# Performance work log

Measured on AMD Instinct MI355X. Metric: run time of the kernel, lower is better.

The kernel has to match this reference:

```python
import jax, jax.numpy as jnp
import numpy as np

N, E, B = 20000, 60000, 800
H = 64          # node_out_feats
EOUT = 64       # edge_out_feats
D = H + EOUT    # set2set input dim = 128
NT = 138        # n_tasks


def _forward(node_feats, edge_feats, fp_vector, src, dst, gid,
             Wn, bn, We1, be1, We2, be2, Wres, Wgx, bgx, Wgh, bgh,
             Wep, bep,
             Wlx0, Wlh0, bl0, Wlx1, Wlh1, bl1, Wlx2, Wlh2, bl2,
             Wfp, bfp, bn_g, bn_b, bn_m, bn_v,
             Wf1, bf1, Wf2, bf2, Wp, bp):
    # ---- CustomMPNNGNN (dgllife MPNNGNN: proj + NNConv(edge-net) + GRU) ----
    h = jax.nn.relu(node_feats @ Wn + bn)                       # [N,64]
    We = jax.nn.relu(edge_feats @ We1 + be1) @ We2 + be2        # [E,4096]
    We = We.reshape(-1, H, H)                                   # [E,64,64] per-edge weight
    hs = h                                                      # GRU hidden state
    for _ in range(3):
        msg = jnp.einsum('ei,eio->eo', h[src], We)              # edge gather + matvec
        agg = jax.ops.segment_sum(msg, dst, num_segments=N)     # scatter-add to dst
        m = jax.nn.relu(agg + h @ Wres)                         # residual root weight
        gx = m @ Wgx + bgx
        gh = hs @ Wgh + bgh
        xr, xz, xn = jnp.split(gx, 3, axis=-1)
        hr, hz, hn = jnp.split(gh, 3, axis=-1)
        r = jax.nn.sigmoid(xr + hr)
        z = jax.nn.sigmoid(xz + hz)
        n = jnp.tanh(xn + r * hn)
        hs = (1.0 - z) * n + z * hs
        h = hs
    # ---- _internal_readout: gather src node emb + projected edge emb, segment-sum at dst ----
    e_emb = jax.nn.relu(edge_feats @ Wep + bep)                 # [E,64]
    src_msg = jnp.concatenate([h[src], e_emb], axis=1)          # [E,128]
    feat = jax.ops.segment_sum(src_msg, dst, num_segments=N)    # [N,128]
    # ---- Set2Set (3-layer LSTM hidden 128, 6 iterations) ----
    q_star = jnp.zeros((B, 2 * D), feat.dtype)
    hc = [(jnp.zeros((B, D), feat.dtype), jnp.zeros((B, D), feat.dtype)) for _ in range(3)]
    lstm = [(Wlx0, Wlh0, bl0), (Wlx1, Wlh1, bl1), (Wlx2, Wlh2, bl2)]
    for _ in range(6):
        x = q_star
        new_hc = []
        for (Wx, Wh, b), (hl, cl) in zip(lstm, hc):
            g = x @ Wx + hl @ Wh + b                            # [B,512] gates i,f,g,o
            gi, gf, gg, go = jnp.split(g, 4, axis=-1)
            cl = jax.nn.sigmoid(gf) * cl + jax.nn.sigmoid(gi) * jnp.tanh(gg)
            hl = jax.nn.sigmoid(go) * jnp.tanh(cl)
            new_hc.append((hl, cl))
            x = hl
        hc = new_hc
        q = x                                                   # [B,128]
        e = jnp.sum(feat * q[gid], axis=-1)                     # [N]
        emax = jax.ops.segment_max(e, gid, num_segments=B)
        a = jnp.exp(e - emax[gid])
        denom = jax.ops.segment_sum(a, gid, num_segments=B)
        alpha = a / (denom[gid] + 1e-9)
        r = jax.ops.segment_sum(alpha[:, None] * feat, gid, num_segments=B)  # [B,128]
        q_star = jnp.concatenate([q, r], axis=1)                # [B,256]
    # ---- Fingerprint encoder: Linear + BatchNorm1d(eval) + ReLU ----
    fp = fp_vector @ Wfp + bfp
    fp = jax.nn.relu((fp - bn_m) * bn_g * jax.lax.rsqrt(bn_v + 1e-5) + bn_b)  # [B,128]
    # ---- combined FFN (384 -> 300 -> 256) + prediction head ----
    comb = jnp.concatenate([q_star, fp], axis=1)                # [B,384]
    emb = jax.nn.relu(comb @ Wf1 + bf1) @ Wf2 + bf2             # [B,256]
    out = jax.nn.relu(emb) @ Wp + bp                            # [B,138]
    return out


def setup_inputs() -> dict:
    key = jax.random.key(0)
    ks = iter(jax.random.split(key, 64))
    def nrm(shape, s):
        return jax.random.normal(next(ks), shape, jnp.float32) * s
    inp = {}
    inp['node_feats'] = jax.random.normal(next(ks), (N, 134), jnp.float32)
    inp['edge_feats'] = jax.random.uniform(next(ks), (E, 6), jnp.float32)
    inp['fp_vector'] = jax.random.uniform(next(ks), (B, 1024), jnp.float32)
    inp['src'] = jax.random.randint(next(ks), (E,), 0, N)
    inp['dst'] = jax.random.randint(next(ks), (E,), 0, N)
    inp['gid'] = jnp.sort(jax.random.randint(next(ks), (N,), 0, B))
    # MPNN params
    inp['Wn'] = nrm((134, H), 0.08); inp['bn'] = jnp.zeros((H,), jnp.float32)
    inp['We1'] = nrm((6, 128), 0.2); inp['be1'] = jnp.zeros((128,), jnp.float32)
    inp['We2'] = nrm((128, H * H), 0.05); inp['be2'] = jnp.zeros((H * H,), jnp.float32)
    inp['Wres'] = nrm((H, H), 0.1)
    inp['Wgx'] = nrm((H, 3 * H), 0.1); inp['bgx'] = jnp.zeros((3 * H,), jnp.float32)
    inp['Wgh'] = nrm((H, 3 * H), 0.1); inp['bgh'] = jnp.zeros((3 * H,), jnp.float32)
    # edge projection for readout
    inp['Wep'] = nrm((6, EOUT), 0.2); inp['bep'] = jnp.zeros((EOUT,), jnp.float32)
    # Set2Set LSTM (layer0 input 2D=256, layers 1-2 input D=128, hidden D=128)
    inp['Wlx0'] = nrm((2 * D, 4 * D), 0.06); inp['Wlh0'] = nrm((D, 4 * D), 0.06); inp['bl0'] = jnp.zeros((4 * D,), jnp.float32)
    inp['Wlx1'] = nrm((D, 4 * D), 0.06); inp['Wlh1'] = nrm((D, 4 * D), 0.06); inp['bl1'] = jnp.zeros((4 * D,), jnp.float32)
    inp['Wlx2'] = nrm((D, 4 * D), 0.06); inp['Wlh2'] = nrm((D, 4 * D), 0.06); inp['bl2'] = jnp.zeros((4 * D,), jnp.float32)
    # fingerprint encoder
    inp['Wfp'] = nrm((1024, 128), 0.03); inp['bfp'] = jnp.zeros((128,), jnp.float32)
    inp['bn_g'] = jnp.ones((128,), jnp.float32); inp['bn_b'] = jnp.zeros((128,), jnp.float32)
    inp['bn_m'] = jnp.zeros((128,), jnp.float32); inp['bn_v'] = jnp.ones((128,), jnp.float32)
    # combined FFN + prediction head
    inp['Wf1'] = nrm((2 * D + 128, 300), 0.06); inp['bf1'] = jnp.zeros((300,), jnp.float32)
    inp['Wf2'] = nrm((300, 256), 0.06); inp['bf2'] = jnp.zeros((256,), jnp.float32)
    inp['Wp'] = nrm((256, NT), 0.06); inp['bp'] = jnp.zeros((NT,), jnp.float32)
    return inp


def reference(node_feats, edge_feats, fp_vector, src, dst, gid,
              Wn, bn, We1, be1, We2, be2, Wres, Wgx, bgx, Wgh, bgh,
              Wep, bep,
              Wlx0, Wlh0, bl0, Wlx1, Wlh1, bl1, Wlx2, Wlh2, bl2,
              Wfp, bfp, bn_g, bn_b, bn_m, bn_v,
              Wf1, bf1, Wf2, bf2, Wp, bp):
    return _forward(node_feats, edge_feats, fp_vector, src, dst, gid,
                    Wn, bn, We1, be1, We2, be2, Wres, Wgx, bgx, Wgh, bgh,
                    Wep, bep,
                    Wlx0, Wlh0, bl0, Wlx1, Wlh1, bl1, Wlx2, Wlh2, bl2,
                    Wfp, bfp, bn_g, bn_b, bn_m, bn_v,
                    Wf1, bf1, Wf2, bf2, Wp, bp)
```

## Files before the change

### kernel.cpp

```cpp
#include <hip/hip_runtime.h>

typedef short short8 __attribute__((ext_vector_type(8)));
typedef float f32x4  __attribute__((ext_vector_type(4)));
typedef unsigned int u32x4 __attribute__((ext_vector_type(4)));
typedef _Float16 f16x2 __attribute__((ext_vector_type(2)));

#define NN 20000
#define NE 60000
#define NB 800
#define NTASK 138
#define EB 128
#define EPAD 60032

#define O_WX0 0
#define O_WH0 131072
#define O_WX1 196608
#define O_WH1 262144
#define O_WX2 327680
#define O_WH2 393216
#define O_WF1 458752
#define O_WF2 573952
#define O_WP  650752
#define NWB   686080

#if defined(__has_builtin)
#if __has_builtin(__builtin_amdgcn_fdot2)
#define HAVE_DOT2 1
#else
#define HAVE_DOT2 0
#endif
#else
#define HAVE_DOT2 0
#endif

static __device__ __forceinline__ float sigm(float x) { return 1.f / (1.f + expf(-x)); }

static __device__ __forceinline__ unsigned short f2bf(float x) {
    unsigned u = __float_as_uint(x);
    unsigned r = (u + 0x7fffu + ((u >> 16) & 1u)) >> 16;
    return (unsigned short)r;
}
static __device__ __forceinline__ float bf2f(unsigned short b) {
    return __uint_as_float(((unsigned)b) << 16);
}

#if HAVE_DOT2
static __device__ __forceinline__ unsigned short f2w(float x) {
    _Float16 h = (_Float16)x;
    return __builtin_bit_cast(unsigned short, h);
}
static __device__ __forceinline__ float w2f(unsigned short s) {
    return (float)__builtin_bit_cast(_Float16, s);
}
static __device__ __forceinline__ unsigned int pack2f16(float a, float b) {
    unsigned short lo = __builtin_bit_cast(unsigned short, (_Float16)a);
    unsigned short hi = __builtin_bit_cast(unsigned short, (_Float16)b);
    return ((unsigned)hi << 16) | lo;
}
#define BC2(u) __builtin_bit_cast(f16x2, (unsigned int)(u))
#else
static __device__ __forceinline__ unsigned short f2w(float x) { return f2bf(x); }
static __device__ __forceinline__ float w2f(unsigned short s) { return bf2f(s); }
#endif

__global__ void kpre(float* __restrict__ zbase, int nz4,
                     const float* __restrict__ We2, const float* __restrict__ be2,
                     unsigned short* __restrict__ thi,
                     const int* __restrict__ gid, int* __restrict__ seg,
                     const float* __restrict__ fpv, const float* __restrict__ Wfp,
                     const float* __restrict__ bfpv,
                     const float* __restrict__ bng, const float* __restrict__ bnb,
                     const float* __restrict__ bnm, const float* __restrict__ bnv,
                     float* __restrict__ fpb,
                     const float* __restrict__ nf, const float* __restrict__ Wn,
                     const float* __restrict__ bn, float* __restrict__ hf,
                     unsigned short* __restrict__ hb,
                     const float* __restrict__ ef, const float* __restrict__ We1,
                     const float* __restrict__ be1, float* __restrict__ xt,
                     const float* __restrict__ Wlx0, const float* __restrict__ Wlh0,
                     const float* __restrict__ Wlx1, const float* __restrict__ Wlh1,
                     const float* __restrict__ Wlx2, const float* __restrict__ Wlh2,
                     const float* __restrict__ Wf1, const float* __restrict__ Wf2,
                     const float* __restrict__ Wp, unsigned short* __restrict__ wb,
                     int B0, int B1, int B2, int B3, int B4, int B5) {
    __shared__ float st[64 * 65];
    __shared__ float sNF[16 * 134];
    __shared__ float sred[128];
    __shared__ float sW[6 * 128];
    __shared__ float sbv[128];
    const int bid = blockIdx.x, tid = threadIdx.x;
    if (bid < B0) {
        long base = (long)bid * 2048 + tid;
        #pragma unroll
        for (int r = 0; r < 8; ++r) {
            long i = base + r * 256;
            if (i < nz4) reinterpret_cast<f32x4*>(zbase)[i] = f32x4{0.f, 0.f, 0.f, 0.f};
        }
    } else if (bid < B1) {
        int c = bid - B0;
        const float* srcp = (c < 128) ? We2 + (long)c * 4096 : be2;
        for (int idx = tid; idx < 4096; idx += 256) {
            int o = idx & 63, i = idx >> 6;
            st[o * 65 + i] = srcp[idx];
        }
        __syncthreads();
        for (int idx = tid; idx < 4096; idx += 256) {
            int i = idx & 63, o = idx >> 6;
            thi[(long)c * 4096 + idx] = f2bf(st[o * 65 + i]);
        }
    } else if (bid < B2) {
        int b = (bid - B1) * 256 + tid;
        if (b <= NB) {
            int lo = 0, hi = NN;
            while (lo < hi) { int mid = (lo + hi) >> 1; if (gid[mid] < b) lo = mid + 1; else hi = mid; }
            seg[b] = lo;
        }
    } else if (bid < B3) {
        int g = bid - B2;
        int u = tid & 127, half = tid >> 7;
        float acc = half ? 0.f : bfpv[u];
        const float* fr = fpv + (long)g * 1024 + half * 512;
        const float* wr = Wfp + (long)half * 512 * 128;
        for (int k = 0; k < 512; ++k) acc += fr[k] * wr[k * 128 + u];
        if (half) sred[u] = acc;
        __syncthreads();
        if (!half) {
            acc += sred[u];
            float sc = bng[u] / sqrtf(bnv[u] + 1e-5f);
            fpb[(long)g * 128 + u] = fmaxf((acc - bnm[u]) * sc + bnb[u], 0.f);
        }
    } else if (bid < B4) {
        int n0 = (bid - B3) * 16;
        const float* nfb = nf + (long)n0 * 134;
        for (int i = tid; i < 16 * 134; i += 256) sNF[i] = nfb[i];
        __syncthreads();
        int u = tid & 63, jg = tid >> 6;
        float a[4];
        float bv = bn[u];
        #pragma unroll
        for (int jj = 0; jj < 4; ++jj) a[jj] = bv;
        for (int k = 0; k < 134; ++k) {
            float w = Wn[k * 64 + u];
            #pragma unroll
            for (int jj = 0; jj < 4; ++jj) a[jj] += sNF[(jg * 4 + jj) * 134 + k] * w;
        }
        #pragma unroll
        for (int jj = 0; jj < 4; ++jj) {
            long o = (long)(n0 + jg * 4 + jj) * 64 + u;
            float v = fmaxf(a[jj], 0.f);
            hf[o] = v;
            hb[o] = f2bf(v);
        }
    } else if (bid < B5) {
        for (int i = tid; i < 768; i += 256) sW[i] = We1[i];
        if (tid < 128) sbv[tid] = be1[tid];
        __syncthreads();
        int e = (bid - B4) * 256 + tid;
        if (e < NE) {
            float e0 = ef[(long)e * 6 + 0], e1 = ef[(long)e * 6 + 1], e2 = ef[(long)e * 6 + 2];
            float e3 = ef[(long)e * 6 + 3], e4 = ef[(long)e * 6 + 4], e5 = ef[(long)e * 6 + 5];
            for (int c = 0; c < 128; ++c) {
                float a = sbv[c];
                a += e0 * sW[c];       a += e1 * sW[128 + c]; a += e2 * sW[256 + c];
                a += e3 * sW[384 + c]; a += e4 * sW[512 + c]; a += e5 * sW[640 + c];
                xt[(long)c * EPAD + e] = fmaxf(a, 0.f);
            }
        } else if (e < EPAD) {
            for (int c = 0; c < 128; ++c) xt[(long)c * EPAD + e] = 0.f;
        }
    } else {
        int t0 = (bid - B5) * 2048 + tid;
        #pragma unroll
        for (int r = 0; r < 8; ++r) {
            int i = t0 + r * 256;
            if (i >= NWB) break;
            float v;
            if (i < O_WF1) {
                const float* srcp; int base;
                if (i < O_WH0)      { srcp = Wlx0; base = O_WX0; }
                else if (i < O_WX1) { srcp = Wlh0; base = O_WH0; }
                else if (i < O_WH1) { srcp = Wlx1; base = O_WX1; }
                else if (i < O_WX2) { srcp = Wlh1; base = O_WH1; }
                else if (i < O_WH2) { srcp = Wlx2; base = O_WX2; }
                else                { srcp = Wlh2; base = O_WH2; }
                int il = i - base;
                int kb = il >> 12, g = (il >> 3) & 511, kk = il & 7;
                v = srcp[(kb * 8 + kk) * 512 + g];
            }
            else if (i < O_WF2) v = Wf1[i - O_WF1];
            else if (i < O_WP)  v = Wf2[i - O_WF2];
            else                v = Wp[i - O_WP];
            wb[i] = f2w(v);
        }
    }
}

__global__ __launch_bounds__(256) void keinsum(
    const unsigned short* __restrict__ hb,
    const float* __restrict__ hf, const float* __restrict__ Wres,
    const float* __restrict__ xt,
    const unsigned short* __restrict__ thi,
    const int* __restrict__ src, const int* __restrict__ dst,
    float* __restrict__ agg) {
    __shared__ __align__(16) unsigned short sB[3 * 64 * 72];
    __shared__ __align__(16) float sX[3 * EB];
    const int bid = blockIdx.x, tid = threadIdx.x;
    if (bid >= 469) {
        int t = (bid - 469) * 256 + tid;
        int u = t & 63;
        int n0 = (t >> 6) * 8;
        if (n0 >= NN) return;
        float a[8] = {0.f, 0.f, 0.f, 0.f, 0.f, 0.f, 0.f, 0.f};
        for (int k = 0; k < 64; ++k) {
            float w = Wres[k * 64 + u];
            #pragma unroll
            for (int j = 0; j < 8; ++j) a[j] += hf[(long)(n0 + j) * 64 + k] * w;
        }
        #pragma unroll
        for (int j = 0; j < 8; ++j) atomicAdd(&agg[(long)(n0 + j) * 64 + u], a[j]);
        return;
    }
    const int lane = tid & 63, wave = tid >> 6;
    const int m = lane & 15, q = lane >> 4;
    const int eb = bid * EB;
    const int e0 = eb + wave * 32;

    short8 ahi[2][2];
    #pragma unroll
    for (int eg = 0; eg < 2; ++eg) {
        int em = e0 + eg * 16 + m; if (em >= NE) em = NE - 1;
        int sn = src[em];
        ahi[eg][0] = *reinterpret_cast<const short8*>(hb + (long)sn * 64 + q * 8);
        ahi[eg][1] = *reinterpret_cast<const short8*>(hb + (long)sn * 64 + 32 + q * 8);
    }
    float msg[2][4][4];
    #pragma unroll
    for (int eg = 0; eg < 2; ++eg)
        #pragma unroll
        for (int nt = 0; nt < 4; ++nt)
            #pragma unroll
            for (int r = 0; r < 4; ++r) msg[eg][nt][r] = 0.f;

    short8 rB0a, rB0b, rB1a, rB1b;
    float rX0, rX1;

    auto GLOAD0 = [&](int c) {
        const unsigned short* bb = thi + (long)c * 4096;
        rB0a = *reinterpret_cast<const short8*>(bb + tid * 8);
        rB0b = *reinterpret_cast<const short8*>(bb + (tid + 256) * 8);
        rX0 = (tid < EB) ? ((c < 128) ? xt[(long)c * EPAD + eb + tid] : 1.f) : 0.f;
    };
    auto GLOAD1 = [&](int c) {
        const unsigned short* bb = thi + (long)c * 4096;
        rB1a = *reinterpret_cast<const short8*>(bb + tid * 8);
        rB1b = *reinterpret_cast<const short8*>(bb + (tid + 256) * 8);
        rX1 = (tid < EB) ? ((c < 128) ? xt[(long)c * EPAD + eb + tid] : 1.f) : 0.f;
    };
    auto DSW0 = [&](int buf) {
        unsigned short* base = &sB[buf * 4608];
        *reinterpret_cast<short8*>(&base[(tid >> 3) * 72 + (tid & 7) * 8]) = rB0a;
        int u = tid + 256;
        *reinterpret_cast<short8*>(&base[(u >> 3) * 72 + (u & 7) * 8]) = rB0b;
        if (tid < EB) sX[buf * EB + tid] = rX0;
    };
    auto DSW1 = [&](int buf) {
        unsigned short* base = &sB[buf * 4608];
        *reinterpret_cast<short8*>(&base[(tid >> 3) * 72 + (tid & 7) * 8]) = rB1a;
        int u = tid + 256;
        *reinterpret_cast<short8*>(&base[(u >> 3) * 72 + (u & 7) * 8]) = rB1b;
        if (tid < EB) sX[buf * EB + tid] = rX1;
    };
    auto CMP = [&](int buf) {
        const unsigned short* base = &sB[buf * 4608];
        f32x4 xw[2];
        #pragma unroll
        for (int eg = 0; eg < 2; ++eg)
            xw[eg] = *reinterpret_cast<const f32x4*>(&sX[buf * EB + wave * 32 + eg * 16 + q * 4]);
        short8 b0[4], b1[4];
        #pragma unroll
        for (int nt = 0; nt < 4; ++nt) {
            const unsigned short* rp = &base[(nt * 16 + m) * 72 + q * 8];
            b0[nt] = *reinterpret_cast<const short8*>(rp);
            b1[nt] = *reinterpret_cast<const short8*>(rp + 32);
        }
        #pragma unroll
        for (int eg = 0; eg < 2; ++eg)
            #pragma unroll
            for (int nt = 0; nt < 4; ++nt) {
                f32x4 z = {0.f, 0.f, 0.f, 0.f};
                z = __builtin_amdgcn_mfma_f32_16x16x32_bf16(ahi[eg][0], b0[nt], z, 0, 0, 0);
                z = __builtin_amdgcn_mfma_f32_16x16x32_bf16(ahi[eg][1], b1[nt], z, 0, 0, 0);
                #pragma unroll
                for (int r = 0; r < 4; ++r) msg[eg][nt][r] += xw[eg][r] * z[r];
            }
    };

    GLOAD0(0);
    DSW0(0);
    GLOAD1(1);
    int c = 0;
    for (; c + 1 < 129; c += 2) {
        int s = c % 3;
        __syncthreads();
        if (c + 2 < 129) GLOAD0(c + 2);
        DSW1((s + 1) % 3);
        CMP(s);
        __syncthreads();
        if (c + 3 < 129) GLOAD1(c + 3);
        if (c + 2 < 129) DSW0((s + 2) % 3);
        CMP((s + 1) % 3);
    }
    if (c < 129) { __syncthreads(); CMP(c % 3); }

    #pragma unroll
    for (int eg = 0; eg < 2; ++eg)
        #pragma unroll
        for (int r = 0; r < 4; ++r) {
            int e = e0 + eg * 16 + q * 4 + r;
            if (e < NE) {
                int d = dst[e];
                #pragma unroll
                for (int nt = 0; nt < 4; ++nt)
                    atomicAdd(&agg[(long)d * 64 + nt * 16 + m], msg[eg][nt][r]);
            }
        }
}

__global__ void kgruz(const float* __restrict__ agg, const float* __restrict__ h,
                      const float* __restrict__ Wgx, const float* __restrict__ bgx,
                      const float* __restrict__ Wgh, const float* __restrict__ bgh,
                      float* __restrict__ hof, unsigned short* __restrict__ hb,
                      float* __restrict__ aggN) {
    const int bid = blockIdx.x, tid = threadIdx.x;
    if (bid >= 625) {
        long base = (long)(bid - 625) * 2048 + tid;
        #pragma unroll
        for (int r = 0; r < 8; ++r) {
            long i = base + r * 256;
            if (i < 320000) reinterpret_cast<f32x4*>(aggN)[i] = f32x4{0.f, 0.f, 0.f, 0.f};
        }
        return;
    }
    __shared__ float sA[2048], sH[2048];
    const int n0 = bid * 32;
    const float* ab = agg + (long)n0 * 64;
    const float* hrow = h + (long)n0 * 64;
    for (int i = tid; i < 2048; i += 256) { sA[i] = ab[i]; sH[i] = hrow[i]; }
    __syncthreads();
    const int u = tid & 63, jg = tid >> 6;
    float xr[8], xz[8], xn[8], hr[8], hz[8], hn[8];
    float b0 = bgx[u], b1 = bgx[64 + u], b2 = bgx[128 + u];
    float d0 = bgh[u], d1 = bgh[64 + u], d2 = bgh[128 + u];
    #pragma unroll
    for (int j = 0; j < 8; ++j) {
        xr[j] = b0; xz[j] = b1; xn[j] = b2;
        hr[j] = d0; hz[j] = d1; hn[j] = d2;
    }
    for (int k = 0; k < 64; ++k) {
        float w0 = Wgx[k * 192 + u], w1 = Wgx[k * 192 + 64 + u], w2 = Wgx[k * 192 + 128 + u];
        float v0 = Wgh[k * 192 + u], v1 = Wgh[k * 192 + 64 + u], v2 = Wgh[k * 192 + 128 + u];
        #pragma unroll
        for (int j = 0; j < 8; ++j) {
            int n = jg * 8 + j;
            float mk = fmaxf(sA[n * 64 + k], 0.f);
            float hk = sH[n * 64 + k];
            xr[j] += mk * w0; xz[j] += mk * w1; xn[j] += mk * w2;
            hr[j] += hk * v0; hz[j] += hk * v1; hn[j] += hk * v2;
        }
    }
    #pragma unroll
    for (int j = 0; j < 8; ++j) {
        int n = jg * 8 + j;
        float rg = sigm(xr[j] + hr[j]);
        float zg = sigm(xz[j] + hz[j]);
        float ng = tanhf(xn[j] + rg * hn[j]);
        long o = (long)(n0 + n) * 64 + u;
        float hv = (1.f - zg) * ng + zg * sH[n * 64 + u];
        hof[o] = hv;
        hb[o] = f2bf(hv);
    }
}

__global__ void kreadout(const float* __restrict__ h,
                         const float* __restrict__ ef, const float* __restrict__ Wep,
                         const float* __restrict__ bep,
                         const int* __restrict__ src, const int* __restrict__ dst,
                         float* __restrict__ feat) {
    int t = blockIdx.x * blockDim.x + threadIdx.x;
    if (t >= NE * 128) return;
    int e = t >> 7, j = t & 127;
    float v;
    if (j < 64) {
        v = h[(long)src[e] * 64 + j];
    } else {
        int o = j - 64;
        v = bep[o];
        #pragma unroll
        for (int k = 0; k < 6; ++k) v += ef[(long)e * 6 + k] * Wep[k * 64 + o];
        v = fmaxf(v, 0.f);
    }
    atomicAdd(&feat[(long)dst[e] * 128 + j], v);
}

__global__ __launch_bounds__(512) void klstmattn(
    const float* __restrict__ feat, const int* __restrict__ seg,
    float* __restrict__ esg,
    const unsigned short* __restrict__ wb,
    const float* __restrict__ bl0, const float* __restrict__ bl1, const float* __restrict__ bl2,
    const float* __restrict__ fpb,
    const float* __restrict__ bf1, const float* __restrict__ bf2, const float* __restrict__ bp,
    float* __restrict__ out) {
    __shared__ float sQ[2][256];
    __shared__ float sHs[3][2][128];
    __shared__ float sCs[3][2][128];
    __shared__ float sG[2][512];
    __shared__ float sE[2][512];
    __shared__ float sH2[2][128];
    __shared__ float sR[2][2][128];
    __shared__ float sred[2][4];
    __shared__ float s1b[2][300];
    __shared__ float s2[2][256];
#if HAVE_DOT2
    __shared__ __align__(16) unsigned int sXp[2][128];
    __shared__ __align__(16) unsigned int sHp[2][64];
#else
    __shared__ float sXH[2][256];
    __shared__ float sHin[2][128];
#endif
    const int tid = threadIdx.x;
    const int b0g = blockIdx.x * 2;
    const unsigned short* Wx[3] = {wb + O_WX0, wb + O_WX1, wb + O_WX2};
    const unsigned short* Wh[3] = {wb + O_WH0, wb + O_WH1, wb + O_WH2};
    const float* bl[3] = {bl0, bl1, bl2};

    const int group = tid >> 8;
    const int t = tid & 255;
    const int wv = t >> 6, lane = t & 63;
    const int j = t & 127, half = t >> 7;
    const int s0 = seg[b0g + group], s1 = seg[b0g + group + 1], len = s1 - s0;

    sQ[tid >> 8][tid & 255] = 0.f;
    {
        float* hp = &sHs[0][0][0];
        float* cp = &sCs[0][0][0];
        for (int i = tid; i < 768; i += 512) { hp[i] = 0.f; cp[i] = 0.f; }
    }
    __syncthreads();

    for (int t6 = 0; t6 < 6; ++t6) {
#if HAVE_DOT2
        if (tid < 256) {
            int b = tid >> 7, u = tid & 127;
            sXp[b][u] = pack2f16(sQ[b][2 * u], sQ[b][2 * u + 1]);
        } else if (tid < 384) {
            int t2 = tid - 256;
            int bb = t2 >> 6, uu = t2 & 63;
            sHp[bb][uu] = pack2f16(sHs[0][bb][2 * uu], sHs[0][bb][2 * uu + 1]);
        }
#else
        {
            int b = tid >> 8, u = tid & 255;
            sXH[b][u] = sQ[b][u];
            if (tid < 256) {
                int bb = tid >> 7, uu = tid & 127;
                sHin[bb][uu] = sHs[0][bb][uu];
            }
        }
#endif
        __syncthreads();

        for (int l = 0; l < 3; ++l) {
            const int Kx = l ? 128 : 256;
            const int g = tid;
            const unsigned short* wxp = Wx[l];
            const unsigned short* whp = Wh[l];
            float bv = bl[l][g];
            float a0 = bv, a1 = bv, a0b = 0.f, a1b = 0.f;
#if HAVE_DOT2
            #pragma unroll 4
            for (int kb = 0; kb < (Kx >> 3); ++kb) {
                u32x4 wu = *reinterpret_cast<const u32x4*>(wxp + ((kb << 9) + g) * 8);
                u32x4 x0 = *reinterpret_cast<const u32x4*>(&sXp[0][kb << 2]);
                u32x4 x1 = *reinterpret_cast<const u32x4*>(&sXp[1][kb << 2]);
                a0  = __builtin_amdgcn_fdot2(BC2(wu[0]), BC2(x0[0]), a0,  false);
                a1  = __builtin_amdgcn_fdot2(BC2(wu[0]), BC2(x1[0]), a1,  false);
                a0b = __builtin_amdgcn_fdot2(BC2(wu[1]), BC2(x0[1]), a0b, false);
                a1b = __builtin_amdgcn_fdot2(BC2(wu[1]), BC2(x1[1]), a1b, false);
                a0  = __builtin_amdgcn_fdot2(BC2(wu[2]), BC2(x0[2]), a0,  false);
                a1  = __builtin_amdgcn_fdot2(BC2(wu[2]), BC2(x1[2]), a1,  false);
                a0b = __builtin_amdgcn_fdot2(BC2(wu[3]), BC2(x0[3]), a0b, false);
                a1b = __builtin_amdgcn_fdot2(BC2(wu[3]), BC2(x1[3]), a1b, false);
            }
            #pragma unroll 4
            for (int kb = 0; kb < 16; ++kb) {
                u32x4 wu = *reinterpret_cast<const u32x4*>(whp + ((kb << 9) + g) * 8);
                u32x4 h0 = *reinterpret_cast<const u32x4*>(&sHp[0][kb << 2]);
                u32x4 h1 = *reinterpret_cast<const u32x4*>(&sHp[1][kb << 2]);
                a0  = __builtin_amdgcn_fdot2(BC2(wu[0]), BC2(h0[0]), a0,  false);
                a1  = __builtin_amdgcn_fdot2(BC2(wu[0]), BC2(h1[0]), a1,  false);
                a0b = __builtin_amdgcn_fdot2(BC2(wu[1]), BC2(h0[1]), a0b, false);
                a1b = __builtin_amdgcn_fdot2(BC2(wu[1]), BC2(h1[1]), a1b, false);
                a0  = __builtin_amdgcn_fdot2(BC2(wu[2]), BC2(h0[2]), a0,  false);
                a1  = __builtin_amdgcn_fdot2(BC2(wu[2]), BC2(h1[2]), a1,  false);
                a0b = __builtin_amdgcn_fdot2(BC2(wu[3]), BC2(h0[3]), a0b, false);
                a1b = __builtin_amdgcn_fdot2(BC2(wu[3]), BC2(h1[3]), a1b, false);
            }
#else
            #pragma unroll 4
            for (int kb = 0; kb < (Kx >> 3); ++kb) {
                short8 wvv = *reinterpret_cast<const short8*>(wxp + ((kb << 9) + g) * 8);
                const f32x4* xp0 = reinterpret_cast<const f32x4*>(&sXH[0][kb << 3]);
                const f32x4* xp1 = reinterpret_cast<const f32x4*>(&sXH[1][kb << 3]);
                f32x4 xa0 = xp0[0], xb0 = xp0[1];
                f32x4 xa1 = xp1[0], xb1 = xp1[1];
                #pragma unroll
                for (int kk = 0; kk < 4; ++kk) {
                    float w0 = w2f((unsigned short)wvv[kk]);
                    float w1 = w2f((unsigned short)wvv[kk + 4]);
                    a0  += xa0[kk] * w0;  a1  += xa1[kk] * w0;
                    a0b += xb0[kk] * w1;  a1b += xb1[kk] * w1;
                }
            }
            #pragma unroll 4
            for (int kb = 0; kb < 16; ++kb) {
                short8 wvv = *reinterpret_cast<const short8*>(whp + ((kb << 9) + g) * 8);
                const f32x4* hp0 = reinterpret_cast<const f32x4*>(&sHin[0][kb << 3]);
                const f32x4* hp1 = reinterpret_cast<const f32x4*>(&sHin[1][kb << 3]);
                f32x4 ha0 = hp0[0], hb0 = hp0[1];
                f32x4 ha1 = hp1[0], hb1 = hp1[1];
                #pragma unroll
                for (int kk = 0; kk < 4; ++kk) {
                    float w0 = w2f((unsigned short)wvv[kk]);
                    float w1 = w2f((unsigned short)wvv[kk + 4]);
                    a0  += ha0[kk] * w0;  a1  += ha1[kk] * w0;
                    a0b += hb0[kk] * w1;  a1b += hb1[kk] * w1;
                }
            }
#endif
            sG[0][g] = a0 + a0b;
            sG[1][g] = a1 + a1b;
            __syncthreads();
            if (tid < 256) {
                int b = tid >> 7, u = tid & 127;
                float gi = sG[b][u], gf = sG[b][128 + u], gg = sG[b][256 + u], go = sG[b][384 + u];
                float c_ = sigm(gf) * sCs[l][b][u] + sigm(gi) * tanhf(gg);
                float h_ = sigm(go) * tanhf(c_);
                sCs[l][b][u] = c_;
                sHs[l][b][u] = h_;
                if (l == 2) sH2[b][u] = h_;
#if HAVE_DOT2
                float hn = __shfl_down(h_, 1, 64);
                if (!(u & 1)) sXp[b][u >> 1] = pack2f16(h_, hn);
#else
                sXH[b][u] = h_;
#endif
            } else if (l < 2) {
                int t2 = tid - 256;
#if HAVE_DOT2
                if (t2 < 128) {
                    int bb = t2 >> 6, uu = t2 & 63;
                    sHp[bb][uu] = pack2f16(sHs[l + 1][bb][2 * uu], sHs[l + 1][bb][2 * uu + 1]);
                }
#else
                int b = t2 >> 7, u = t2 & 127;
                sHin[b][u] = sHs[l + 1][b][u];
#endif
            }
            __syncthreads();
        }

        for (int idx = wv; idx < len; idx += 4) {
            long n = s0 + idx;
            float p = feat[n * 128 + lane] * sH2[group][lane]
                    + feat[n * 128 + 64 + lane] * sH2[group][64 + lane];
            for (int off = 32; off; off >>= 1) p += __shfl_down(p, off, 64);
            if (lane == 0) { if (idx < 512) sE[group][idx] = p; else esg[n] = p; }
        }
        __syncthreads();
        auto ev = [&](int i) { return i < 512 ? sE[group][i] : esg[s0 + i]; };
        float lm = -1e30f;
        for (int i = t; i < len; i += 256) lm = fmaxf(lm, ev(i));
        for (int off = 32; off; off >>= 1) lm = fmaxf(lm, __shfl_down(lm, off, 64));
        if (lane == 0) sred[group][wv] = lm;
        __syncthreads();
        float mx = fmaxf(fmaxf(sred[group][0], sred[group][1]),
                         fmaxf(sred[group][2], sred[group][3]));
        __syncthreads();
        float ls = 0.f;
        for (int i = t; i < len; i += 256) {
            float e_ = expf(ev(i) - mx);
            if (i < 512) sE[group][i] = e_; else esg[s0 + i] = e_;
            ls += e_;
        }
        for (int off = 32; off; off >>= 1) ls += __shfl_down(ls, off, 64);
        if (lane == 0) sred[group][wv] = ls;
        __syncthreads();
        float inv = 1.f / (sred[group][0] + sred[group][1] + sred[group][2] + sred[group][3] + 1e-9f);
        float r0 = 0.f, r1 = 0.f;
        {
            int i = half;
            for (; i + 2 < len; i += 4) {
                r0 += ev(i) * feat[(long)(s0 + i) * 128 + j];
                r1 += ev(i + 2) * feat[(long)(s0 + i + 2) * 128 + j];
            }
            for (; i < len; i += 2)
                r0 += ev(i) * feat[(long)(s0 + i) * 128 + j];
        }
        sR[group][half][j] = r0 + r1;
        __syncthreads();
        float rr = (sR[group][0][j] + sR[group][1][j]) * inv;
        if (half == 0) {
            sQ[group][j] = sH2[group][j];
            sQ[group][128 + j] = rr;
        }

        if (t6 == 5) {
            __syncthreads();
            if (half == 0) {
                sE[group][j] = sH2[group][j];
                sE[group][128 + j] = rr;
            } else {
                sE[group][256 + j] = fpb[(long)(b0g + group) * 128 + j];
            }
            __syncthreads();
            const unsigned short* Wf1b = wb + O_WF1;
            const unsigned short* Wf2b = wb + O_WF2;
            const unsigned short* Wpb  = wb + O_WP;
            for (int task = tid; task < 600; task += 512) {
                int g = task / 300, u = task % 300;
                float acc = bf1[u];
                for (int k = 0; k < 384; ++k) acc += sE[g][k] * w2f(Wf1b[k * 300 + u]);
                s1b[g][u] = fmaxf(acc, 0.f);
            }
            __syncthreads();
            for (int task = tid; task < 512; task += 512) {
                int g = task >> 8, u = task & 255;
                float acc = bf2[u];
                for (int k = 0; k < 300; ++k) acc += s1b[g][k] * w2f(Wf2b[k * 256 + u]);
                s2[g][u] = fmaxf(acc, 0.f);
            }
            __syncthreads();
            for (int task = tid; task < 2 * NTASK; task += 512) {
                int g = task / NTASK, u = task % NTASK;
                float acc = bp[u];
                for (int k = 0; k < 256; ++k) acc += s2[g][k] * w2f(Wpb[k * NTASK + u]);
                out[(long)(b0g + g) * NTASK + u] = acc;
            }
        } else {
            __syncthreads();
        }
    }
}

extern "C" void kernel_launch(void* const* d_in, const int* in_sizes, int n_in,
                              void* d_out, int out_size, void* d_ws, size_t ws_size,
                              hipStream_t stream) {
    auto fp_ = [&](int i) { return (const float*)d_in[i]; };
    auto ip_ = [&](int i) { return (const int*)d_in[i]; };
    const float *nf = fp_(0), *ef = fp_(1), *fpv = fp_(2);
    const int *src = ip_(3), *dst = ip_(4), *gid = ip_(5);
    const float *Wn = fp_(6), *bn = fp_(7), *We1 = fp_(8), *be1 = fp_(9);
    const float *We2 = fp_(10), *be2 = fp_(11), *Wres = fp_(12);
    const float *Wgx = fp_(13), *bgx = fp_(14), *Wgh = fp_(15), *bgh = fp_(16);
    const float *Wep = fp_(17), *bep = fp_(18);
    const float *Wlx0 = fp_(19), *Wlh0 = fp_(20), *bl0 = fp_(21);
    const float *Wlx1 = fp_(22), *Wlh1 = fp_(23), *bl1 = fp_(24);
    const float *Wlx2 = fp_(25), *Wlh2 = fp_(26), *bl2 = fp_(27);
    const float *Wfp = fp_(28), *bfpv = fp_(29);
    const float *bng = fp_(30), *bnb = fp_(31), *bnm = fp_(32), *bnv = fp_(33);
    const float *Wf1 = fp_(34), *bf1 = fp_(35), *Wf2 = fp_(36), *bf2 = fp_(37);
    const float *Wp = fp_(38), *bp = fp_(39);

    char* w = (char*)d_ws;
    auto alloc = [&](size_t bytes) -> char* {
        char* p = w; w += (bytes + 255) & ~(size_t)255; return p;
    };
    float* hA = (float*)alloc((size_t)NN * 64 * 4);
    float* hB = (float*)alloc((size_t)NN * 64 * 4);
    unsigned short* hbA = (unsigned short*)alloc((size_t)NN * 64 * 2);
    unsigned short* hbB = (unsigned short*)alloc((size_t)NN * 64 * 2);
    unsigned short* we2thi = (unsigned short*)alloc((size_t)129 * 4096 * 2);
    unsigned short* wbf = (unsigned short*)alloc((size_t)NWB * 2);
    float* aggB = (float*)alloc((size_t)NN * 64 * 4);
    char* zstart = w;
    float* aggA  = (float*)alloc((size_t)NN * 64 * 4);
    float* feat  = (float*)alloc((size_t)NN * 128 * 4);
    size_t zfloats = (size_t)(w - zstart) / 4;
    float* es   = (float*)alloc((size_t)NN * 4);
    int*   seg  = (int*)alloc((size_t)(NB + 1) * 4);
    float* fpb  = (float*)alloc((size_t)NB * 128 * 4);
    float* xt   = (float*)alloc((size_t)128 * EPAD * 4);

    int nz4 = (int)(zfloats / 4);
    int zb  = (nz4 + 2047) / 2048;
    int B0 = zb;
    int B1 = B0 + 129;
    int B2 = B1 + 4;
    int B3 = B2 + NB;
    int B4 = B3 + 1250;
    int B5 = B4 + 235;
    int B6 = B5 + (NWB + 2047) / 2048;
    kpre<<<B6, 256, 0, stream>>>((float*)zstart, nz4, We2, be2, we2thi, gid, seg,
                                 fpv, Wfp, bfpv, bng, bnb, bnm, bnv, fpb,
                                 nf, Wn, bn, hA, hbA,
                                 ef, We1, be1, xt,
                                 Wlx0, Wlh0, Wlx1, Wlh1, Wlx2, Wlh2, Wf1, Wf2, Wp, wbf,
                                 B0, B1, B2, B3, B4, B5);

    float* hf[2] = {hA, hB};
    unsigned short* hb[2] = {hbA, hbB};
    float* aggbuf[2] = {aggA, aggB};
    int cur = 0;
    for (int it = 0; it < 3; ++it) {
        float* agg  = aggbuf[it & 1];
        float* aggN = aggbuf[1 - (it & 1)];
        keinsum<<<469 + 625, 256, 0, stream>>>(hb[cur], hf[cur], Wres,
                                               xt, we2thi, src, dst, agg);
        kgruz<<<625 + 157, 256, 0, stream>>>(agg, hf[cur], Wgx, bgx, Wgh, bgh,
                                             hf[1 - cur], hb[1 - cur], aggN);
        cur = 1 - cur;
    }
    kreadout<<<(NE * 128 + 255) / 256, 256, 0, stream>>>(hf[cur], ef, Wep, bep, src, dst, feat);

    klstmattn<<<NB / 2, 512, 0, stream>>>(feat, seg, es, wbf, bl0, bl1, bl2,
                                          fpb, bf1, bf2, bp, (float*)d_out);
}
```

Baseline: 861.6 us.

## Process one graph per block in Set2Set LSTM kernel instead of two

The Set2Set LSTM/attention kernel now handles one graph per 512-thread block and launches NB blocks instead of NB/2. Each thread computes one gate for a single graph with four independent fdot2 accumulators, and the attention readout splits nodes across 8 waves / 4 row-quarters. This doubles the grid to spread the sequential LSTM chain over more CUs. The cost is that each LSTM weight load now serves one graph instead of two, doubling weight traffic per graph.

```diff
diff --git a/kernel.cpp b/kernel.cpp
--- a/kernel.cpp
+++ b/kernel.cpp
@@ -410,62 +410,52 @@
     const float* __restrict__ fpb,
     const float* __restrict__ bf1, const float* __restrict__ bf2, const float* __restrict__ bp,
     float* __restrict__ out) {
-    __shared__ float sQ[2][256];
-    __shared__ float sHs[3][2][128];
-    __shared__ float sCs[3][2][128];
-    __shared__ float sG[2][512];
-    __shared__ float sE[2][512];
-    __shared__ float sH2[2][128];
-    __shared__ float sR[2][2][128];
-    __shared__ float sred[2][4];
-    __shared__ float s1b[2][300];
-    __shared__ float s2[2][256];
+    __shared__ float sQ[256];
+    __shared__ float sHs[3][128];
+    __shared__ float sCs[3][128];
+    __shared__ float sG[512];
+    __shared__ float sE[512];
+    __shared__ float sH2[128];
+    __shared__ float sR[4][128];
+    __shared__ float sred[8];
+    __shared__ float s1b[300];
+    __shared__ float s2[256];
 #if HAVE_DOT2
-    __shared__ __align__(16) unsigned int sXp[2][128];
-    __shared__ __align__(16) unsigned int sHp[2][64];
-#else
-    __shared__ float sXH[2][256];
-    __shared__ float sHin[2][128];
+    __shared__ __align__(16) unsigned int sXp[128];
+    __shared__ __align__(16) unsigned int sHp[64];
+#else
+    __shared__ float sXH[256];
+    __shared__ float sHin[128];
 #endif
     const int tid = threadIdx.x;
-    const int b0g = blockIdx.x * 2;
+    const int g0 = blockIdx.x;
     const unsigned short* Wx[3] = {wb + O_WX0, wb + O_WX1, wb + O_WX2};
     const unsigned short* Wh[3] = {wb + O_WH0, wb + O_WH1, wb + O_WH2};
     const float* bl[3] = {bl0, bl1, bl2};
 
-    const int group = tid >> 8;
-    const int t = tid & 255;
-    const int wv = t >> 6, lane = t & 63;
-    const int j = t & 127, half = t >> 7;
-    const int s0 = seg[b0g + group], s1 = seg[b0g + group + 1], len = s1 - s0;
-
-    sQ[tid >> 8][tid & 255] = 0.f;
+    const int wv = tid >> 6, lane = tid & 63;
+    const int j = tid & 127, q4 = tid >> 7;
+    const int s0 = seg[g0], s1 = seg[g0 + 1], len = s1 - s0;
+
+    if (tid < 256) sQ[tid] = 0.f;
     {
-        float* hp = &sHs[0][0][0];
-        float* cp = &sCs[0][0][0];
-        for (int i = tid; i < 768; i += 512) { hp[i] = 0.f; cp[i] = 0.f; }
+        float* hp = &sHs[0][0];
+        float* cp = &sCs[0][0];
+        if (tid < 384) { hp[tid] = 0.f; cp[tid] = 0.f; }
     }
     __syncthreads();
 
     for (int t6 = 0; t6 < 6; ++t6) {
 #if HAVE_DOT2
-        if (tid < 256) {
-            int b = tid >> 7, u = tid & 127;
-            sXp[b][u] = pack2f16(sQ[b][2 * u], sQ[b][2 * u + 1]);
-        } else if (tid < 384) {
-            int t2 = tid - 256;
-            int bb = t2 >> 6, uu = t2 & 63;
-            sHp[bb][uu] = pack2f16(sHs[0][bb][2 * uu], sHs[0][bb][2 * uu + 1]);
-        }
-#else
-        {
-            int b = tid >> 8, u = tid & 255;
-            sXH[b][u] = sQ[b][u];
-            if (tid < 256) {
-                int bb = tid >> 7, uu = tid & 127;
-                sHin[bb][uu] = sHs[0][bb][uu];
-            }
-        }
+        if (tid < 128) {
+            sXp[tid] = pack2f16(sQ[2 * tid], sQ[2 * tid + 1]);
+        } else if (tid < 192) {
+            int uu = tid - 128;
+            sHp[uu] = pack2f16(sHs[0][2 * uu], sHs[0][2 * uu + 1]);
+        }
+#else
+        if (tid < 256) sXH[tid] = sQ[tid];
+        else if (tid < 384) sHin[tid - 256] = sHs[0][tid - 256];
 #endif
         __syncthreads();
 
@@ -474,177 +464,150 @@
             const int g = tid;
             const unsigned short* wxp = Wx[l];
             const unsigned short* whp = Wh[l];
-            float bv = bl[l][g];
-            float a0 = bv, a1 = bv, a0b = 0.f, a1b = 0.f;
+            float a0 = bl[l][g], a1 = 0.f, a2 = 0.f, a3 = 0.f;
 #if HAVE_DOT2
-            #pragma unroll 4
+            #pragma unroll 8
             for (int kb = 0; kb < (Kx >> 3); ++kb) {
                 u32x4 wu = *reinterpret_cast<const u32x4*>(wxp + ((kb << 9) + g) * 8);
-                u32x4 x0 = *reinterpret_cast<const u32x4*>(&sXp[0][kb << 2]);
-                u32x4 x1 = *reinterpret_cast<const u32x4*>(&sXp[1][kb << 2]);
-                a0  = __builtin_amdgcn_fdot2(BC2(wu[0]), BC2(x0[0]), a0,  false);
-                a1  = __builtin_amdgcn_fdot2(BC2(wu[0]), BC2(x1[0]), a1,  false);
-                a0b = __builtin_amdgcn_fdot2(BC2(wu[1]), BC2(x0[1]), a0b, false);
-                a1b = __builtin_amdgcn_fdot2(BC2(wu[1]), BC2(x1[1]), a1b, false);
-                a0  = __builtin_amdgcn_fdot2(BC2(wu[2]), BC2(x0[2]), a0,  false);
-                a1  = __builtin_amdgcn_fdot2(BC2(wu[2]), BC2(x1[2]), a1,  false);
-                a0b = __builtin_amdgcn_fdot2(BC2(wu[3]), BC2(x0[3]), a0b, false);
-                a1b = __builtin_amdgcn_fdot2(BC2(wu[3]), BC2(x1[3]), a1b, false);
-            }
-            #pragma unroll 4
+                u32x4 x0 = *reinterpret_cast<const u32x4*>(&sXp[kb << 2]);
+                a0 = __builtin_amdgcn_fdot2(BC2(wu[0]), BC2(x0[0]), a0, false);
+                a1 = __builtin_amdgcn_fdot2(BC2(wu[1]), BC2(x0[1]), a1, false);
+                a2 = __builtin_amdgcn_fdot2(BC2(wu[2]), BC2(x0[2]), a2, false);
+                a3 = __builtin_amdgcn_fdot2(BC2(wu[3]), BC2(x0[3]), a3, false);
+            }
+            #pragma unroll 8
             for (int kb = 0; kb < 16; ++kb) {
                 u32x4 wu = *reinterpret_cast<const u32x4*>(whp + ((kb << 9) + g) * 8);
-                u32x4 h0 = *reinterpret_cast<const u32x4*>(&sHp[0][kb << 2]);
-                u32x4 h1 = *reinterpret_cast<const u32x4*>(&sHp[1][kb << 2]);
-                a0  = __builtin_amdgcn_fdot2(BC2(wu[0]), BC2(h0[0]), a0,  false);
-                a1  = __builtin_amdgcn_fdot2(BC2(wu[0]), BC2(h1[0]), a1,  false);
-                a0b = __builtin_amdgcn_fdot2(BC2(wu[1]), BC2(h0[1]), a0b, false);
-                a1b = __builtin_amdgcn_fdot2(BC2(wu[1]), BC2(h1[1]), a1b, false);
-                a0  = __builtin_amdgcn_fdot2(BC2(wu[2]), BC2(h0[2]), a0,  false);
-                a1  = __builtin_amdgcn_fdot2(BC2(wu[2]), BC2(h1[2]), a1,  false);
-                a0b = __builtin_amdgcn_fdot2(BC2(wu[3]), BC2(h0[3]), a0b, false);
-                a1b = __builtin_amdgcn_fdot2(BC2(wu[3]), BC2(h1[3]), a1b, false);
-            }
-#else
-            #pragma unroll 4
+                u32x4 h0 = *reinterpret_cast<const u32x4*>(&sHp[kb << 2]);
+                a0 = __builtin_amdgcn_fdot2(BC2(wu[0]), BC2(h0[0]), a0, false);
+                a1 = __builtin_amdgcn_fdot2(BC2(wu[1]), BC2(h0[1]), a1, false);
+                a2 = __builtin_amdgcn_fdot2(BC2(wu[2]), BC2(h0[2]), a2, false);
+                a3 = __builtin_amdgcn_fdot2(BC2(wu[3]), BC2(h0[3]), a3, false);
+            }
+#else
+            #pragma unroll 8
             for (int kb = 0; kb < (Kx >> 3); ++kb) {
                 short8 wvv = *reinterpret_cast<const short8*>(wxp + ((kb << 9) + g) * 8);
-                const f32x4* xp0 = reinterpret_cast<const f32x4*>(&sXH[0][kb << 3]);
-                const f32x4* xp1 = reinterpret_cast<const f32x4*>(&sXH[1][kb << 3]);
-                f32x4 xa0 = xp0[0], xb0 = xp0[1];
-                f32x4 xa1 = xp1[0], xb1 = xp1[1];
+                const f32x4* xp0 = reinterpret_cast<const f32x4*>(&sXH[kb << 3]);
+                f32x4 xa = xp0[0], xb = xp0[1];
                 #pragma unroll
                 for (int kk = 0; kk < 4; ++kk) {
-                    float w0 = w2f((unsigned short)wvv[kk]);
-                    float w1 = w2f((unsigned short)wvv[kk + 4]);
-                    a0  += xa0[kk] * w0;  a1  += xa1[kk] * w0;
-                    a0b += xb0[kk] * w1;  a1b += xb1[kk] * w1;
+                    a0 += xa[kk] * w2f((unsigned short)wvv[kk]);
+                    a1 += xb[kk] * w2f((unsigned short)wvv[kk + 4]);
                 }
             }
-            #pragma unroll 4
+            #pragma unroll 8
             for (int kb = 0; kb < 16; ++kb) {
                 short8 wvv = *reinterpret_cast<const short8*>(whp + ((kb << 9) + g) * 8);
-                const f32x4* hp0 = reinterpret_cast<const f32x4*>(&sHin[0][kb << 3]);
-                const f32x4* hp1 = reinterpret_cast<const f32x4*>(&sHin[1][kb << 3]);
-                f32x4 ha0 = hp0[0], hb0 = hp0[1];
-                f32x4 ha1 = hp1[0], hb1 = hp1[1];
+                const f32x4* hp0 = reinterpret_cast<const f32x4*>(&sHin[kb << 3]);
+                f32x4 ha = hp0[0], hbv = hp0[1];
                 #pragma unroll
                 for (int kk = 0; kk < 4; ++kk) {
-                    float w0 = w2f((unsigned short)wvv[kk]);
-                    float w1 = w2f((unsigned short)wvv[kk + 4]);
-                    a0  += ha0[kk] * w0;  a1  += ha1[kk] * w0;
-                    a0b += hb0[kk] * w1;  a1b += hb1[kk] * w1;
+                    a0 += ha[kk] * w2f((unsigned short)wvv[kk]);
+                    a1 += hbv[kk] * w2f((unsigned short)wvv[kk + 4]);
                 }
             }
 #endif
-            sG[0][g] = a0 + a0b;
-            sG[1][g] = a1 + a1b;
+            sG[g] = (a0 + a1) + (a2 + a3);
             __syncthreads();
-            if (tid < 256) {
-                int b = tid >> 7, u = tid & 127;
-                float gi = sG[b][u], gf = sG[b][128 + u], gg = sG[b][256 + u], go = sG[b][384 + u];
-                float c_ = sigm(gf) * sCs[l][b][u] + sigm(gi) * tanhf(gg);
+            if (tid < 128) {
+                int u = tid;
+                float gi = sG[u], gf = sG[128 + u], gg = sG[256 + u], go = sG[384 + u];
+                float c_ = sigm(gf) * sCs[l][u] + sigm(gi) * tanhf(gg);
                 float h_ = sigm(go) * tanhf(c_);
-                sCs[l][b][u] = c_;
-                sHs[l][b][u] = h_;
-                if (l == 2) sH2[b][u] = h_;
+                sCs[l][u] = c_;
+                sHs[l][u] = h_;
+                if (l == 2) sH2[u] = h_;
 #if HAVE_DOT2
                 float hn = __shfl_down(h_, 1, 64);
-                if (!(u & 1)) sXp[b][u >> 1] = pack2f16(h_, hn);
-#else
-                sXH[b][u] = h_;
+                if (!(u & 1)) sXp[u >> 1] = pack2f16(h_, hn);
+#else
+                sXH[u] = h_;
 #endif
             } else if (l < 2) {
-                int t2 = tid - 256;
 #if HAVE_DOT2
-                if (t2 < 128) {
-                    int bb = t2 >> 6, uu = t2 & 63;
-                    sHp[bb][uu] = pack2f16(sHs[l + 1][bb][2 * uu], sHs[l + 1][bb][2 * uu + 1]);
+                if (tid < 192) {
+                    int uu = tid - 128;
+                    sHp[uu] = pack2f16(sHs[l + 1][2 * uu], sHs[l + 1][2 * uu + 1]);
                 }
 #else
-                int b = t2 >> 7, u = t2 & 127;
-                sHin[b][u] = sHs[l + 1][b][u];
+                if (tid < 256) sHin[tid - 128] = sHs[l + 1][tid - 128];
 #endif
             }
             __syncthreads();
         }
 
-        for (int idx = wv; idx < len; idx += 4) {
+        for (int idx = wv; idx < len; idx += 8) {
             long n = s0 + idx;
-            float p = feat[n * 128 + lane] * sH2[group][lane]
-                    + feat[n * 128 + 64 + lane] * sH2[group][64 + lane];
+            float p = feat[n * 128 + lane] * sH2[lane]
+                    + feat[n * 128 + 64 + lane] * sH2[64 + lane];
             for (int off = 32; off; off >>= 1) p += __shfl_down(p, off, 64);
-            if (lane == 0) { if (idx < 512) sE[group][idx] = p; else esg[n] = p; }
-        }
-        __syncthreads();
-        auto ev = [&](int i) { return i < 512 ? sE[group][i] : esg[s0 + i]; };
+            if (lane == 0) { if (idx < 512) sE[idx] = p; else esg[n] = p; }
+        }
+        __syncthreads();
+        auto ev = [&](int i) { return i < 512 ? sE[i] : esg[s0 + i]; };
         float lm = -1e30f;
-        for (int i = t; i < len; i += 256) lm = fmaxf(lm, ev(i));
+        for (int i = tid; i < len; i += 512) lm = fmaxf(lm, ev(i));
         for (int off = 32; off; off >>= 1) lm = fmaxf(lm, __shfl_down(lm, off, 64));
-        if (lane == 0) sred[group][wv] = lm;
-        __syncthreads();
-        float mx = fmaxf(fmaxf(sred[group][0], sred[group][1]),
-                         fmaxf(sred[group][2], sred[group][3]));
+        if (lane == 0) sred[wv] = lm;
+        __syncthreads();
+        float mx = fmaxf(fmaxf(fmaxf(sred[0], sred[1]), fmaxf(sred[2], sred[3])),
+                         fmaxf(fmaxf(sred[4], sred[5]), fmaxf(sred[6], sred[7])));
         __syncthreads();
         float ls = 0.f;
-        for (int i = t; i < len; i += 256) {
+        for (int i = tid; i < len; i += 512) {
             float e_ = expf(ev(i) - mx);
-            if (i < 512) sE[group][i] = e_; else esg[s0 + i] = e_;
+            if (i < 512) sE[i] = e_; else esg[s0 + i] = e_;
             ls += e_;
         }
         for (int off = 32; off; off >>= 1) ls += __shfl_down(ls, off, 64);
-        if (lane == 0) sred[group][wv] = ls;
-        __syncthreads();
-        float inv = 1.f / (sred[group][0] + sred[group][1] + sred[group][2] + sred[group][3] + 1e-9f);
+        if (lane == 0) sred[wv] = ls;
+        __syncthreads();
+        float inv = 1.f / (((sred[0] + sred[1]) + (sred[2] + sred[3]))
+                         + ((sred[4] + sred[5]) + (sred[6] + sred[7])) + 1e-9f);
         float r0 = 0.f, r1 = 0.f;
         {
-            int i = half;
-            for (; i + 2 < len; i += 4) {
+            int i = q4;
+            for (; i + 4 < len; i += 8) {
                 r0 += ev(i) * feat[(long)(s0 + i) * 128 + j];
-                r1 += ev(i + 2) * feat[(long)(s0 + i + 2) * 128 + j];
-            }
-            for (; i < len; i += 2)
+                r1 += ev(i + 4) * feat[(long)(s0 + i + 4) * 128 + j];
+            }
+            for (; i < len; i += 4)
                 r0 += ev(i) * feat[(long)(s0 + i) * 128 + j];
         }
-        sR[group][half][j] = r0 + r1;
-        __syncthreads();
-        float rr = (sR[group][0][j] + sR[group][1][j]) * inv;
-        if (half == 0) {
-            sQ[group][j] = sH2[group][j];
-            sQ[group][128 + j] = rr;
+        sR[q4][j] = r0 + r1;
+        __syncthreads();
+        float rr = ((sR[0][j] + sR[1][j]) + (sR[2][j] + sR[3][j])) * inv;
+        if (q4 == 0) {
+            sQ[j] = sH2[j];
+            sQ[128 + j] = rr;
         }
 
         if (t6 == 5) {
             __syncthreads();
-            if (half == 0) {
-                sE[group][j] = sH2[group][j];
-                sE[group][128 + j] = rr;
-            } else {
-                sE[group][256 + j] = fpb[(long)(b0g + group) * 128 + j];
-            }
+            if (q4 == 0)      sE[j] = sH2[j];
+            else if (q4 == 1) sE[128 + j] = rr;
+            else if (q4 == 2) sE[256 + j] = fpb[(long)g0 * 128 + j];
             __syncthreads();
             const unsigned short* Wf1b = wb + O_WF1;
             const unsigned short* Wf2b = wb + O_WF2;
             const unsigned short* Wpb  = wb + O_WP;
-            for (int task = tid; task < 600; task += 512) {
-                int g = task / 300, u = task % 300;
+            for (int u = tid; u < 300; u += 512) {
                 float acc = bf1[u];
-                for (int k = 0; k < 384; ++k) acc += sE[g][k] * w2f(Wf1b[k * 300 + u]);
-                s1b[g][u] = fmaxf(acc, 0.f);
+                for (int k = 0; k < 384; ++k) acc += sE[k] * w2f(Wf1b[k * 300 + u]);
+                s1b[u] = fmaxf(acc, 0.f);
             }
             __syncthreads();
-            for (int task = tid; task < 512; task += 512) {
-                int g = task >> 8, u = task & 255;
+            for (int u = tid; u < 256; u += 512) {
                 float acc = bf2[u];
-                for (int k = 0; k < 300; ++k) acc += s1b[g][k] * w2f(Wf2b[k * 256 + u]);
-                s2[g][u] = fmaxf(acc, 0.f);
+                for (int k = 0; k < 300; ++k) acc += s1b[k] * w2f(Wf2b[k * 256 + u]);
+                s2[u] = fmaxf(acc, 0.f);
             }
             __syncthreads();
-            for (int task = tid; task < 2 * NTASK; task += 512) {
-                int g = task / NTASK, u = task % NTASK;
+            for (int u = tid; u < NTASK; u += 512) {
                 float acc = bp[u];
-                for (int k = 0; k < 256; ++k) acc += s2[g][k] * w2f(Wpb[k * NTASK + u]);
-                out[(long)(b0g + g) * NTASK + u] = acc;
+                for (int k = 0; k < 256; ++k) acc += s2[k] * w2f(Wpb[k * NTASK + u]);
+                out[(long)g0 * NTASK + u] = acc;
             }
         } else {
             __syncthreads();
@@ -722,6 +685,6 @@
     }
     kreadout<<<(NE * 128 + 255) / 256, 256, 0, stream>>>(hf[cur], ef, Wep, bep, src, dst, feat);
 
-    klstmattn<<<NB / 2, 512, 0, stream>>>(feat, seg, es, wbf, bl0, bl1, bl2,
-                                          fpb, bf1, bf2, bp, (float*)d_out);
-}
+    klstmattn<<<NB, 512, 0, stream>>>(feat, seg, es, wbf, bl0, bl1, bl2,
+                                      fpb, bf1, bf2, bp, (float*)d_out);
+}
```

New measurement: 1.047 ms. 21.5% more time.
